# Kernel optimization log

Measured on AMD Instinct MI355X. Metric: run time of the kernel, lower is better.

Reference implementation:

```python
import jax, jax.numpy as jnp
import numpy as np

THRESHOLD = 10.0
K = 24
EPS = 1e-9
BN_EPS = 1e-5


def setup_inputs() -> dict:
    key = jax.random.key(0)
    k0, k1, k2, k3 = jax.random.split(key, 4)
    B, C, H, W = 4, 256, 64, 64
    x = jax.random.normal(k0, (B, C, H, W), jnp.float32)
    fc_w = jax.random.normal(k1, (C, C), jnp.float32) * (1.0 / np.sqrt(C))
    fc_b = jax.random.normal(k2, (C,), jnp.float32) * 0.01
    dist_w = jax.random.normal(k3, (64, C), jnp.float32) * (1.0 / np.sqrt(C))
    bn_gamma = jnp.ones((C,), jnp.float32)
    bn_beta = jnp.zeros((C,), jnp.float32)
    return {"x": x, "fc_w": fc_w, "fc_b": fc_b, "dist_w": dist_w,
            "bn_gamma": bn_gamma, "bn_beta": bn_beta}


def reference(x, fc_w, fc_b, dist_w, bn_gamma, bn_beta):
    B, C, H, W = x.shape
    N = H * W
    # ds branch: only triggers when H == 40; here H=64 so ds=1 (no pool/interp)
    x_flat = x.reshape(B, C, N).transpose(0, 2, 1)        # [B, N, C]
    # dist_embed: 1x1 conv == linear projection per spatial location
    emb = jnp.einsum('bnc,ec->bne', x_flat, dist_w)       # [B, N, 64]
    # pairwise Euclidean distances (cdist)
    sq = jnp.sum(emb * emb, axis=-1)                      # [B, N]
    d2 = sq[:, :, None] + sq[:, None, :] - 2.0 * jnp.einsum('bne,bme->bnm', emb, emb)
    dist = jnp.sqrt(jnp.clip(d2, 0.0))                    # [B, N, N]
    # kNN mask via top_k of -dist
    _, idx = jax.lax.top_k(-dist, K)                      # [B, N, K]
    bi = jnp.arange(B)[:, None, None]
    ni = jnp.arange(N)[None, :, None]
    knn_mask = jnp.zeros((B, N, N), bool).at[bi, ni, idx].set(True)
    adj = knn_mask & (dist <= THRESHOLD)
    adj = adj | jnp.eye(N, dtype=bool)[None]
    adj_f = adj.astype(x.dtype)                           # H: [B, N, E=N]
    # HypConv: X' = Dv^{-1} H De^{-1} H^T (X Theta), residual added outside
    X_lin = x_flat @ fc_w.T + fc_b                        # [B, N, C]
    Dv = jnp.clip(jnp.sum(adj_f, axis=2), EPS, None)      # [B, N]
    De = jnp.clip(jnp.sum(adj_f, axis=1), EPS, None)      # [B, E]
    H_De_inv = adj_f / De[:, None, :]
    S = (H_De_inv @ adj_f.transpose(0, 2, 1)) / Dv[:, :, None]   # [B, N, N]
    out_flat = S @ X_lin + x_flat                         # residual
    out = out_flat.transpose(0, 2, 1).reshape(B, C, H, W)
    # BatchNorm2d in training mode (batch statistics, biased variance)
    mean = jnp.mean(out, axis=(0, 2, 3))
    var = jnp.var(out, axis=(0, 2, 3))
    o = (out - mean[None, :, None, None]) * jax.lax.rsqrt(var[None, :, None, None] + BN_EPS)
    o = o * bn_gamma[None, :, None, None] + bn_beta[None, :, None, None]
    # SiLU
    return o * jax.nn.sigmoid(o)
```

## Files before the change

kernel.cpp:

```cpp
#include <hip/hip_runtime.h>

#define NB 4096
#define BATCH 4
#define CD 256
#define ED 64
#define KNN 24

typedef __attribute__((ext_vector_type(8))) short bf16x8;
typedef __attribute__((ext_vector_type(4))) float f32x4;

__device__ __forceinline__ unsigned short f2bf(float x) {
  unsigned u = __float_as_uint(x);
  unsigned r = (u + 0x7fffu + ((u >> 16) & 1u)) >> 16;
  return (unsigned short)r;
}

__global__ __launch_bounds__(256) void k_emb(const float* __restrict__ x,
                                             const float* __restrict__ dist_w,
                                             unsigned* __restrict__ emb_hl,
                                             float* __restrict__ sq,
                                             unsigned* __restrict__ thr_g) {
  __shared__ float wds[ED * CD];
  __shared__ float red[64 * 4];
  const int b = blockIdx.x >> 6;
  const int n0 = (blockIdx.x & 63) << 6;
  const int tid = threadIdx.x;
  const float4* wsrc = (const float4*)dist_w;
  float4* wdst = (float4*)wds;
#pragma unroll
  for (int k = 0; k < 16; ++k) wdst[tid + 256 * k] = wsrc[tid + 256 * k];
  __syncthreads();
  const int eg = tid >> 6;
  const int nl = tid & 63;
  const int n = n0 + nl;
  float acc[16];
#pragma unroll
  for (int t = 0; t < 16; ++t) acc[t] = 0.f;
  const float* xb = x + (size_t)b * CD * NB + n;
#pragma unroll 2
  for (int c4 = 0; c4 < CD; c4 += 4) {
    float x0 = xb[(size_t)(c4 + 0) * NB];
    float x1 = xb[(size_t)(c4 + 1) * NB];
    float x2 = xb[(size_t)(c4 + 2) * NB];
    float x3 = xb[(size_t)(c4 + 3) * NB];
#pragma unroll
    for (int t = 0; t < 16; ++t) {
      float4 wv = *(const float4*)&wds[(eg * 16 + t) * CD + c4];
      acc[t] = fmaf(x0, wv.x, acc[t]);
      acc[t] = fmaf(x1, wv.y, acc[t]);
      acc[t] = fmaf(x2, wv.z, acc[t]);
      acc[t] = fmaf(x3, wv.w, acc[t]);
    }
  }
  float s = 0.f;
#pragma unroll
  for (int t = 0; t < 16; ++t) s = fmaf(acc[t], acc[t], s);
  unsigned hw[8], lw[8];
#pragma unroll
  for (int i = 0; i < 8; ++i) {
    unsigned short h0 = f2bf(acc[2 * i]);
    unsigned short h1 = f2bf(acc[2 * i + 1]);
    float l0f = acc[2 * i] - __uint_as_float((unsigned)h0 << 16);
    float l1f = acc[2 * i + 1] - __uint_as_float((unsigned)h1 << 16);
    hw[i] = (unsigned)h0 | ((unsigned)h1 << 16);
    lw[i] = (unsigned)f2bf(l0f) | ((unsigned)f2bf(l1f) << 16);
  }
  uint4* g = (uint4*)emb_hl;
  const size_t gb = ((size_t)(b * NB + n)) * 16;
  const int k15 = n & 15;
  g[gb + ((2 * eg) ^ k15)]     = make_uint4(hw[0], hw[1], hw[2], hw[3]);
  g[gb + ((2 * eg + 1) ^ k15)] = make_uint4(hw[4], hw[5], hw[6], hw[7]);
  g[gb + ((8 + 2 * eg) ^ k15)]     = make_uint4(lw[0], lw[1], lw[2], lw[3]);
  g[gb + ((8 + 2 * eg + 1) ^ k15)] = make_uint4(lw[4], lw[5], lw[6], lw[7]);
  red[nl * 4 + eg] = s;
  __syncthreads();
  if (tid < 64) {
    sq[b * NB + n0 + tid] = red[tid * 4] + red[tid * 4 + 1] + red[tid * 4 + 2] + red[tid * 4 + 3];
    thr_g[(b << 12) + n0 + tid] = 0x42C80000u;
  }
}

__global__ __launch_bounds__(256) void k_wsplit(const float* __restrict__ fc_w,
                                                unsigned* __restrict__ w_hl) {
  const int u = blockIdx.x * 256 + threadIdx.x;
  const int c = u >> 5, cg = u & 31;
  const int kt = cg >> 3, chl = cg & 7;
  const float* src = fc_w + (size_t)c * CD + kt * 64 + chl * 8;
  unsigned hi[4], lo[4];
#pragma unroll
  for (int j = 0; j < 4; ++j) {
    float a0 = src[2 * j], a1 = src[2 * j + 1];
    unsigned short h0 = f2bf(a0), h1 = f2bf(a1);
    float l0 = a0 - __uint_as_float((unsigned)h0 << 16);
    float l1 = a1 - __uint_as_float((unsigned)h1 << 16);
    hi[j] = (unsigned)h0 | ((unsigned)h1 << 16);
    lo[j] = (unsigned)f2bf(l0) | ((unsigned)f2bf(l1) << 16);
  }
  uint4* dst = (uint4*)w_hl;
  const int base = (c * 4 + kt) * 16;
  const int k15 = c & 15;
  dst[base + (chl ^ k15)] = make_uint4(hi[0], hi[1], hi[2], hi[3]);
  dst[base + ((chl + 8) ^ k15)] = make_uint4(lo[0], lo[1], lo[2], lo[3]);
}

__global__ __launch_bounds__(512) void k_xlin(const float* __restrict__ x,
                                              const unsigned* __restrict__ w_hl,
                                              const float* __restrict__ fc_b,
                                              float* __restrict__ xlin) {
  __shared__ __align__(16) unsigned char smem[49152];
  float* xt = (float*)smem;
  unsigned* xhl = (unsigned*)(smem + 16384);
  unsigned* whl = (unsigned*)(smem + 32768);
  const int bid = blockIdx.x;
  const int ct = bid & 3;
  const int nt = (bid >> 2) & 63;
  const int b = bid >> 8;
  const int n0 = nt << 6;
  const int tid = threadIdx.x;
  const int w = tid >> 6, lane = tid & 63;
  const int quad = lane >> 4, lr = lane & 15;
  const int rt = w >> 1;
  const int ct0 = (w & 1) * 2;
  const int rowA = rt * 16 + lr;
  const int cvt_n = tid & 63, cvt_k8 = tid >> 6;
  uint4* whl4 = (uint4*)whl;
  uint4* xhl4 = (uint4*)xhl;
  const uint4* wg = (const uint4*)w_hl;
  f32x4 acc0 = {0.f, 0.f, 0.f, 0.f};
  f32x4 acc1 = {0.f, 0.f, 0.f, 0.f};

#pragma unroll 1
  for (int kt = 0; kt < 4; ++kt) {
    __syncthreads();
#pragma unroll
    for (int i = 0; i < 8; ++i) {
      int idx = tid + 512 * i;
      int k = idx >> 6, n = idx & 63;
      xt[k * 64 + n] = x[((size_t)(b * CD + kt * 64 + k)) * NB + n0 + n];
    }
#pragma unroll
    for (int i = 0; i < 2; ++i) {
      int idx = tid + 512 * i;
      int r = idx >> 4, ch = idx & 15;
      whl4[r * 16 + ch] = wg[(size_t)((ct * 64 + r) * 4 + kt) * 16 + ch];
    }
    __syncthreads();
    {
      unsigned hi[4], lo[4];
#pragma unroll
      for (int j = 0; j < 4; ++j) {
        float a0 = xt[(cvt_k8 * 8 + 2 * j) * 64 + cvt_n];
        float a1 = xt[(cvt_k8 * 8 + 2 * j + 1) * 64 + cvt_n];
        unsigned short h0 = f2bf(a0), h1 = f2bf(a1);
        float l0 = a0 - __uint_as_float((unsigned)h0 << 16);
        float l1 = a1 - __uint_as_float((unsigned)h1 << 16);
        hi[j] = (unsigned)h0 | ((unsigned)h1 << 16);
        lo[j] = (unsigned)f2bf(l0) | ((unsigned)f2bf(l1) << 16);
      }
      const int k15 = cvt_n & 15;
      xhl4[cvt_n * 16 + (cvt_k8 ^ k15)] = make_uint4(hi[0], hi[1], hi[2], hi[3]);
      xhl4[cvt_n * 16 + ((cvt_k8 + 8) ^ k15)] = make_uint4(lo[0], lo[1], lo[2], lo[3]);
    }
    __syncthreads();
#pragma unroll
    for (int kk = 0; kk < 2; ++kk) {
      const int cb = quad + 4 * kk;
      bf16x8 a_hi = *(const bf16x8*)&xhl[rowA * 64 + ((cb) ^ lr) * 4];
      bf16x8 a_lo = *(const bf16x8*)&xhl[rowA * 64 + ((cb + 8) ^ lr) * 4];
      int rowB0 = ct0 * 16 + lr, rowB1 = rowB0 + 16;
      bf16x8 b0_hi = *(const bf16x8*)&whl[rowB0 * 64 + ((cb) ^ lr) * 4];
      bf16x8 b0_lo = *(const bf16x8*)&whl[rowB0 * 64 + ((cb + 8) ^ lr) * 4];
      bf16x8 b1_hi = *(const bf16x8*)&whl[rowB1 * 64 + ((cb) ^ lr) * 4];
      bf16x8 b1_lo = *(const bf16x8*)&whl[rowB1 * 64 + ((cb + 8) ^ lr) * 4];
      acc0 = __builtin_amdgcn_mfma_f32_16x16x32_bf16(a_hi, b0_hi, acc0, 0, 0, 0);
      acc0 = __builtin_amdgcn_mfma_f32_16x16x32_bf16(a_hi, b0_lo, acc0, 0, 0, 0);
      acc0 = __builtin_amdgcn_mfma_f32_16x16x32_bf16(a_lo, b0_hi, acc0, 0, 0, 0);
      acc1 = __builtin_amdgcn_mfma_f32_16x16x32_bf16(a_hi, b1_hi, acc1, 0, 0, 0);
      acc1 = __builtin_amdgcn_mfma_f32_16x16x32_bf16(a_hi, b1_lo, acc1, 0, 0, 0);
      acc1 = __builtin_amdgcn_mfma_f32_16x16x32_bf16(a_lo, b1_hi, acc1, 0, 0, 0);
    }
  }
#pragma unroll
  for (int reg = 0; reg < 4; ++reg) {
    int n = n0 + rt * 16 + quad * 4 + reg;
    float* dst = xlin + ((size_t)(b * NB + n)) * CD + ct * 64;
    int c0 = ct0 * 16 + lr;
    dst[c0] = acc0[reg] + fc_b[ct * 64 + c0];
    dst[c0 + 16] = acc1[reg] + fc_b[ct * 64 + c0 + 16];
  }
}

__global__ __launch_bounds__(512, 4) void k_distp(const unsigned* __restrict__ emb_hl,
                                                  const float* __restrict__ sq,
                                                  unsigned* __restrict__ thr_g,
                                                  unsigned long long* __restrict__ part) {
  __shared__ __align__(16) unsigned char smem[78592];
  unsigned* eN = (unsigned*)smem;
  unsigned* eM = (unsigned*)(smem + 16384);
  float* sqN   = (float*)(smem + 32768);
  float* sqMp  = (float*)(smem + 33024);
  int* hist    = (int*)(smem + 35072);
  int* collectK= (int*)(smem + 51456);
  int* cnt     = (int*)(smem + 51712);
  unsigned long long* cand = (unsigned long long*)(smem + 51968);

  const int bid = blockIdx.x;
  const int mp = bid & 7;
  const int nt = (bid >> 3) & 63;
  const int b  = bid >> 9;
  const int n0 = nt << 6;
  const int m00 = mp << 9;
  const int tid = threadIdx.x;
  const uint4* embg = (const uint4*)emb_hl;
  const size_t bbase = (size_t)b * NB;
  const int gbase = (b << 12) + n0;

#pragma unroll
  for (int k = 0; k < 2; ++k) {
    int q = tid + 512 * k;
    int r = q >> 4, ch = q & 15;
    *(uint4*)&eN[r * 64 + ch * 4] = embg[(bbase + n0 + r) * 16 + ch];
  }
  if (tid < 64) sqN[tid] = sq[b * NB + n0 + tid];
  sqMp[tid] = sq[b * NB + m00 + tid];
#pragma unroll
  for (int i = 0; i < 8; ++i) hist[tid + 512 * i] = 0;

  const int w = tid >> 6, lane = tid & 63;
  const int quad = lane >> 4, lr = lane & 15;
  const int rt = w >> 1;
  const int ct0 = (w & 1) * 2;
  const int rowA = rt * 16 + lr;
  const int rA = tid >> 4, chA = tid & 15;
  const int rB = rA + 32;

  uint4 pf0, pf1;

#define CHUNK_MFMA(m0_)                                                            \
  f32x4 acc0 = {0.f, 0.f, 0.f, 0.f};                                               \
  f32x4 acc1 = {0.f, 0.f, 0.f, 0.f};                                               \
  _Pragma("unroll")                                                                \
  for (int kk = 0; kk < 2; ++kk) {                                                 \
    const int cb = quad + 4 * kk;                                                  \
    bf16x8 a_hi = *(const bf16x8*)&eN[rowA * 64 + ((cb) ^ lr) * 4];                \
    bf16x8 a_lo = *(const bf16x8*)&eN[rowA * 64 + ((cb + 8) ^ lr) * 4];            \
    int rowB0 = ct0 * 16 + lr, rowB1 = rowB0 + 16;                                 \
    bf16x8 b0_hi = *(const bf16x8*)&eM[rowB0 * 64 + ((cb) ^ lr) * 4];              \
    bf16x8 b0_lo = *(const bf16x8*)&eM[rowB0 * 64 + ((cb + 8) ^ lr) * 4];          \
    bf16x8 b1_hi = *(const bf16x8*)&eM[rowB1 * 64 + ((cb) ^ lr) * 4];              \
    bf16x8 b1_lo = *(const bf16x8*)&eM[rowB1 * 64 + ((cb + 8) ^ lr) * 4];          \
    acc0 = __builtin_amdgcn_mfma_f32_16x16x32_bf16(a_hi, b0_hi, acc0, 0, 0, 0);    \
    acc0 = __builtin_amdgcn_mfma_f32_16x16x32_bf16(a_hi, b0_lo, acc0, 0, 0, 0);    \
    acc0 = __builtin_amdgcn_mfma_f32_16x16x32_bf16(a_lo, b0_hi, acc0, 0, 0, 0);    \
    acc1 = __builtin_amdgcn_mfma_f32_16x16x32_bf16(a_hi, b1_hi, acc1, 0, 0, 0);    \
    acc1 = __builtin_amdgcn_mfma_f32_16x16x32_bf16(a_hi, b1_lo, acc1, 0, 0, 0);    \
    acc1 = __builtin_amdgcn_mfma_f32_16x16x32_bf16(a_lo, b1_hi, acc1, 0, 0, 0);    \
  }

#define STAGE_FIRST()                                                \
  pf0 = embg[(bbase + m00 + rA) * 16 + chA];                         \
  pf1 = embg[(bbase + m00 + rB) * 16 + chA];                         \
  *(uint4*)&eM[rA * 64 + chA * 4] = pf0;                             \
  *(uint4*)&eM[rB * 64 + chA * 4] = pf1;                             \
  pf0 = embg[(bbase + m00 + 64 + rA) * 16 + chA];                    \
  pf1 = embg[(bbase + m00 + 64 + rB) * 16 + chA];

#define RESTAGE(ci_, m0_)                                            \
  if ((ci_) < 7) {                                                   \
    *(uint4*)&eM[rA * 64 + chA * 4] = pf0;                           \
    *(uint4*)&eM[rB * 64 + chA * 4] = pf1;                           \
    if ((ci_) < 6) {                                                 \
      pf0 = embg[(bbase + m00 + (m0_) + 128 + rA) * 16 + chA];       \
      pf1 = embg[(bbase + m00 + (m0_) + 128 + rB) * 16 + chA];       \
    }                                                                \
  }

  STAGE_FIRST()
#pragma unroll 1
  for (int ci = 0; ci < 8; ++ci) {
    const int m0 = ci << 6;
    __syncthreads();
    CHUNK_MFMA(m0)
#pragma unroll
    for (int reg = 0; reg < 4; ++reg) {
      int row = rt * 16 + quad * 4 + reg;
      int c0 = ct0 * 16 + lr, c1 = c0 + 16;
      float d20 = fmaxf(sqN[row] + sqMp[m0 + c0] - 2.f * acc0[reg], 0.f);
      float d21 = fmaxf(sqN[row] + sqMp[m0 + c1] - 2.f * acc1[reg], 0.f);
      if (__float_as_uint(d20) <= 0x42C80000u) {
        int bk0 = min(63, (int)(d20 * 0.64f));
        atomicAdd(&hist[bk0 * 64 + row], 1);
      }
      if (__float_as_uint(d21) <= 0x42C80000u) {
        int bk1 = min(63, (int)(d21 * 0.64f));
        atomicAdd(&hist[bk1 * 64 + row], 1);
      }
    }
    __syncthreads();
    RESTAGE(ci, m0)
  }

  if (tid < 64) {
    int cum = 0, kb = 63;
#pragma unroll 1
    for (int k2 = 0; k2 < 64; ++k2) {
      cum += hist[k2 * 64 + tid];
      if (cum >= 24) { kb = k2; break; }
    }
    float edge = (float)(kb + 2) * 1.5625f;
    atomicMin(&thr_g[gbase + tid], __float_as_uint(edge));
    unsigned tg = thr_g[gbase + tid];
    int kImp = min(63, (int)(__uint_as_float(tg) * 0.64f));
    collectK[tid] = min(kb, kImp);
    cnt[tid] = 0;
  }
#pragma unroll
  for (int i = 0; i < 7; ++i) {
    int q = tid + 512 * i;
    if (q < 64 * 52) cand[q] = ~0ULL;
  }
  __syncthreads();

  STAGE_FIRST()
#pragma unroll 1
  for (int ci = 0; ci < 8; ++ci) {
    const int m0 = ci << 6;
    __syncthreads();
    CHUNK_MFMA(m0)
#pragma unroll
    for (int reg = 0; reg < 4; ++reg) {
      int row = rt * 16 + quad * 4 + reg;
      int c0 = ct0 * 16 + lr, c1 = c0 + 16;
      float d20 = fmaxf(sqN[row] + sqMp[m0 + c0] - 2.f * acc0[reg], 0.f);
      float d21 = fmaxf(sqN[row] + sqMp[m0 + c1] - 2.f * acc1[reg], 0.f);
      int kc = collectK[row];
      unsigned bi0 = __float_as_uint(d20), bi1 = __float_as_uint(d21);
      int bk0 = min(63, (int)(d20 * 0.64f));
      int bk1 = min(63, (int)(d21 * 0.64f));
      if (bk0 <= kc && bi0 <= 0x42C80000u) {
        int pos = atomicAdd(&cnt[row], 1);
        if (pos < 52) cand[row * 52 + pos] = ((unsigned long long)bi0 << 32) | (unsigned)(m00 + m0 + c0);
      }
      if (bk1 <= kc && bi1 <= 0x42C80000u) {
        int pos = atomicAdd(&cnt[row], 1);
        if (pos < 52) cand[row * 52 + pos] = ((unsigned long long)bi1 << 32) | (unsigned)(m00 + m0 + c1);
      }
    }
    __syncthreads();
    RESTAGE(ci, m0)
  }
  __syncthreads();

  {
    const int row8 = tid >> 3, sub = tid & 7;
    unsigned long long last = 0;
    unsigned long long* op = part + ((size_t)bid * 64 + row8) * 24;
#pragma unroll 1
    for (int k = 0; k < 24; ++k) {
      unsigned long long lm = ~0ULL;
#pragma unroll
      for (int j2 = 0; j2 < 7; ++j2) {
        int p2 = sub + 8 * j2;
        if (p2 < 52) {
          unsigned long long v2 = cand[row8 * 52 + p2];
          if ((k == 0 || v2 > last) && v2 < lm) lm = v2;
        }
      }
#pragma unroll
      for (int s2 = 1; s2 < 8; s2 <<= 1) {
        unsigned long long o2 = __shfl_xor(lm, s2);
        if (o2 < lm) lm = o2;
      }
      if (sub == 0) op[k] = lm;
      last = lm;
    }
  }
}

__global__ __launch_bounds__(64) void k_merge(const unsigned long long* __restrict__ part,
                                              int* __restrict__ row_idx,
                                              int* __restrict__ row_cnt,
                                              int* __restrict__ col_cnt) {
  const int row = blockIdx.x * 64 + threadIdx.x;
  const int b = row >> 12;
  const int n = row & 4095;
  const int nt = n >> 6, r = n & 63;
  const size_t gb = (size_t)(((b << 6) | nt) << 3);
  unsigned long long h[8];
  int pp[8];
#pragma unroll
  for (int t = 0; t < 8; ++t) {
    h[t] = part[((gb + t) * 64 + r) * 24];
    pp[t] = 0;
  }
  int cnt = 0;
  const int base = row * KNN;
  for (int k = 0; k < 24; ++k) {
    int bs = 0;
    unsigned long long mv = h[0];
#pragma unroll
    for (int t = 1; t < 8; ++t)
      if (h[t] < mv) { mv = h[t]; bs = t; }
    if ((unsigned)(mv >> 32) > 0x42C80000u) break;
    int mi = (int)(mv & 0xFFFFFFFFu);
    row_idx[base + cnt] = mi;
    atomicAdd(&col_cnt[(b << 12) + mi], 1);
    ++cnt;
    int np = ++pp[bs];
    h[bs] = (np < 24) ? part[((gb + bs) * 64 + r) * 24 + np] : ~0ULL;
  }
  row_cnt[row] = cnt;
#pragma unroll 4
  for (int j = cnt; j < 24; ++j) row_idx[base + j] = n;
}

__global__ __launch_bounds__(256) void k_scan(const int* __restrict__ col_cnt,
                                              int* __restrict__ col_start,
                                              int* __restrict__ col_cursor) {
  __shared__ int part[256];
  const int tid = threadIdx.x;
  const int base = tid * 64;
  int s = 0;
  for (int j = 0; j < 64; ++j) s += col_cnt[base + j];
  part[tid] = s;
  __syncthreads();
  for (int off = 1; off < 256; off <<= 1) {
    int v = (tid >= off) ? part[tid - off] : 0;
    __syncthreads();
    part[tid] += v;
    __syncthreads();
  }
  int run = part[tid] - s;
  for (int j = 0; j < 64; ++j) {
    col_start[base + j] = run;
    col_cursor[base + j] = run;
    run += col_cnt[base + j];
  }
}

__global__ __launch_bounds__(64) void k_fill(const int* __restrict__ row_idx,
                                             const int* __restrict__ row_cnt,
                                             int* __restrict__ col_cursor,
                                             int* __restrict__ col_list) {
  const int row = blockIdx.x * 64 + threadIdx.x;
  const int b = row >> 12;
  const int cnt = row_cnt[row];
  for (int j = 0; j < cnt; ++j) {
    int m = row_idx[row * KNN + j];
    int pos = atomicAdd(&col_cursor[(b << 12) + m], 1);
    col_list[pos] = row & 4095;
  }
}

__global__ __launch_bounds__(256) void k_yd(const float* __restrict__ xlin,
                                            const int* __restrict__ col_cnt,
                                            const int* __restrict__ col_start,
                                            const int* __restrict__ col_list,
                                            float* __restrict__ yd) {
  const int le = threadIdx.x >> 6;
  const int c4 = threadIdx.x & 63;
  const int be = blockIdx.x * 4 + le;
  const int b = be >> 12;
  const int deg = col_cnt[be];
  const int start = col_start[be];
  float4 acc = make_float4(0.f, 0.f, 0.f, 0.f);
  int j = 0;
  for (; j + 3 < deg; j += 4) {
    int ma = col_list[start + j], mb2 = col_list[start + j + 1];
    int mc = col_list[start + j + 2], md = col_list[start + j + 3];
    float4 va = *(const float4*)&xlin[(((size_t)(b << 12) + ma) << 8) + c4 * 4];
    float4 vb = *(const float4*)&xlin[(((size_t)(b << 12) + mb2) << 8) + c4 * 4];
    float4 vc = *(const float4*)&xlin[(((size_t)(b << 12) + mc) << 8) + c4 * 4];
    float4 vd = *(const float4*)&xlin[(((size_t)(b << 12) + md) << 8) + c4 * 4];
    acc.x += (va.x + vb.x) + (vc.x + vd.x);
    acc.y += (va.y + vb.y) + (vc.y + vd.y);
    acc.z += (va.z + vb.z) + (vc.z + vd.z);
    acc.w += (va.w + vb.w) + (vc.w + vd.w);
  }
  for (; j < deg; ++j) {
    int m = col_list[start + j];
    float4 v = *(const float4*)&xlin[(((size_t)(b << 12) + m) << 8) + c4 * 4];
    acc.x += v.x; acc.y += v.y; acc.z += v.z; acc.w += v.w;
  }
  float inv = 1.f / (float)deg;
  acc.x *= inv; acc.y *= inv; acc.z *= inv; acc.w *= inv;
  *(float4*)&yd[((size_t)be << 8) + c4 * 4] = acc;
}

__global__ __launch_bounds__(256) void k_out2(const float* __restrict__ yd,
                                              const int* __restrict__ row_idx,
                                              const int* __restrict__ row_cnt,
                                              float* __restrict__ outf) {
  const int b = blockIdx.x >> 8;
  const int nt = blockIdx.x & 255;
  const int le = threadIdx.x >> 6;
  const int c4 = threadIdx.x & 63;
  for (int ii = 0; ii < 4; ++ii) {
    int n = nt * 16 + le * 4 + ii;
    int row = (b << 12) + n;
    int cnt = row_cnt[row];
    int idx[24];
    const int4* ip = (const int4*)(row_idx + (size_t)row * KNN);
#pragma unroll
    for (int t = 0; t < 6; ++t) {
      int4 v = ip[t];
      idx[4 * t] = v.x; idx[4 * t + 1] = v.y; idx[4 * t + 2] = v.z; idx[4 * t + 3] = v.w;
    }
    float4 acc = make_float4(0.f, 0.f, 0.f, 0.f);
#pragma unroll
    for (int j = 0; j < 24; ++j) {
      float wgt = (j < cnt) ? 1.f : 0.f;
      float4 v = *(const float4*)&yd[(((size_t)(b << 12) + idx[j]) << 8) + c4 * 4];
      acc.x = fmaf(wgt, v.x, acc.x);
      acc.y = fmaf(wgt, v.y, acc.y);
      acc.z = fmaf(wgt, v.z, acc.z);
      acc.w = fmaf(wgt, v.w, acc.w);
    }
    float inv = 1.f / (float)cnt;
    acc.x *= inv; acc.y *= inv; acc.z *= inv; acc.w *= inv;
    *(float4*)&outf[((size_t)row << 8) + c4 * 4] = acc;
  }
}

__global__ __launch_bounds__(256) void k_res_bn(const float* __restrict__ x,
                                                float* __restrict__ outf,
                                                float* __restrict__ bn_sum,
                                                float* __restrict__ bn_sumsq) {
  __shared__ float xt[256 * 69];
  const int b = blockIdx.x >> 6;
  const int n0 = (blockIdx.x & 63) << 6;
  const int tid = threadIdx.x;
#pragma unroll 4
  for (int k = 0; k < 16; ++k) {
    int q = tid + 256 * k;
    int c = q >> 4, f = q & 15;
    float4 v = *(const float4*)&x[((size_t)(b * CD + c)) * NB + n0 + 4 * f];
    xt[c * 69 + 4 * f + 0] = v.x;
    xt[c * 69 + 4 * f + 1] = v.y;
    xt[c * 69 + 4 * f + 2] = v.z;
    xt[c * 69 + 4 * f + 3] = v.w;
  }
  __syncthreads();
  float s = 0.f, q = 0.f;
  const size_t rbase = ((size_t)((b << 12) + n0)) << 8;
#pragma unroll 4
  for (int i = 0; i < 64; ++i) {
    float v = outf[rbase + (size_t)i * 256 + tid] + xt[tid * 69 + i];
    outf[rbase + (size_t)i * 256 + tid] = v;
    s += v;
    q = fmaf(v, v, q);
  }
  atomicAdd(&bn_sum[tid], s);
  atomicAdd(&bn_sumsq[tid], q);
}

__global__ __launch_bounds__(256) void k_write(const float* __restrict__ outf,
                                               const float* __restrict__ bn_sum,
                                               const float* __restrict__ bn_sumsq,
                                               const float* __restrict__ gamma,
                                               const float* __restrict__ beta,
                                               float* __restrict__ out) {
  __shared__ float tile[64 * 257];
  __shared__ float sc[256], sh[256];
  const int b = blockIdx.x >> 6;
  const int n0 = (blockIdx.x & 63) << 6;
  const int tid = threadIdx.x;
  {
    const float inv = 1.f / 16384.f;
    float mean = bn_sum[tid] * inv;
    float var = bn_sumsq[tid] * inv - mean * mean;
    float scf = gamma[tid] * rsqrtf(var + 1e-5f);
    sc[tid] = scf;
    sh[tid] = beta[tid] - mean * scf;
  }
  __syncthreads();
#pragma unroll 4
  for (int i = 0; i < 64; ++i) {
    int idx = tid + 256 * i;
    int n = idx >> 8, c = idx & 255;
    float v = outf[(((size_t)(b << 12) + n0 + n) << 8) + c];
    v = fmaf(v, sc[c], sh[c]);
    float w = v / (1.f + expf(-v));
    tile[n * 257 + c] = w;
  }
  __syncthreads();
  const int nl = tid & 63;
  const int cg = tid >> 6;
#pragma unroll 4
  for (int j = 0; j < 64; ++j) {
    int c = cg * 64 + j;
    out[((size_t)(b * CD + c)) * NB + n0 + nl] = tile[nl * 257 + c];
  }
}

extern "C" void kernel_launch(void* const* d_in, const int* in_sizes, int n_in,
                              void* d_out, int out_size, void* d_ws, size_t ws_size,
                              hipStream_t stream) {
  const float* x      = (const float*)d_in[0];
  const float* fc_w   = (const float*)d_in[1];
  const float* fc_b   = (const float*)d_in[2];
  const float* dist_w = (const float*)d_in[3];
  const float* gamma  = (const float*)d_in[4];
  const float* beta   = (const float*)d_in[5];
  float* out = (float*)d_out;
  char* ws = (char*)d_ws;

  const size_t OFF_EHL   = 0;
  const size_t OFF_XLIN  = (size_t)4 << 20;
  const size_t OFF_YD    = (size_t)20 << 20;
  const size_t OFF_OUTF  = (size_t)36 << 20;
  const size_t OFF_SQ    = (size_t)52 << 20;
  const size_t OFF_RIDX  = OFF_SQ + 65536;
  const size_t OFF_RCNT  = OFF_RIDX + 1572864;
  const size_t OFF_CCNT  = OFF_RCNT + 65536;
  const size_t OFF_CSTART = OFF_CCNT + 65536;
  const size_t OFF_CCUR  = OFF_CSTART + 65536;
  const size_t OFF_CLIST = OFF_CCUR + 65536;
  const size_t OFF_BNS   = OFF_CLIST + 1572864;
  const size_t OFF_BNQ   = OFF_BNS + 1024;
  const size_t OFF_THRG  = OFF_BNQ + 1024;
  const size_t OFF_WHL   = OFF_THRG + 65536;
  const size_t TOTAL = OFF_WHL + 262144;
  if (ws_size < TOTAL) return;

  unsigned* emb_hl = (unsigned*)(ws + OFF_EHL);
  float* xlin  = (float*)(ws + OFF_XLIN);
  float* yd    = (float*)(ws + OFF_YD);
  float* outf  = (float*)(ws + OFF_OUTF);
  unsigned long long* part = (unsigned long long*)(ws + OFF_YD);
  float* sq    = (float*)(ws + OFF_SQ);
  int* row_idx = (int*)(ws + OFF_RIDX);
  int* row_cnt = (int*)(ws + OFF_RCNT);
  int* col_cnt = (int*)(ws + OFF_CCNT);
  int* col_start = (int*)(ws + OFF_CSTART);
  int* col_cursor = (int*)(ws + OFF_CCUR);
  int* col_list = (int*)(ws + OFF_CLIST);
  float* bn_sum = (float*)(ws + OFF_BNS);
  float* bn_sumsq = (float*)(ws + OFF_BNQ);
  unsigned* thr_g = (unsigned*)(ws + OFF_THRG);
  unsigned* w_hl = (unsigned*)(ws + OFF_WHL);

  hipMemsetAsync(col_cnt, 0, 65536, stream);
  hipMemsetAsync(bn_sum, 0, 2048, stream);

  k_emb<<<256, 256, 0, stream>>>(x, dist_w, emb_hl, sq, thr_g);
  k_wsplit<<<32, 256, 0, stream>>>(fc_w, w_hl);
  k_xlin<<<1024, 512, 0, stream>>>(x, w_hl, fc_b, xlin);
  k_distp<<<2048, 512, 0, stream>>>(emb_hl, sq, thr_g, part);
  k_merge<<<256, 64, 0, stream>>>(part, row_idx, row_cnt, col_cnt);
  k_scan<<<1, 256, 0, stream>>>(col_cnt, col_start, col_cursor);
  k_fill<<<256, 64, 0, stream>>>(row_idx, row_cnt, col_cursor, col_list);
  k_yd<<<4096, 256, 0, stream>>>(xlin, col_cnt, col_start, col_list, yd);
  k_out2<<<1024, 256, 0, stream>>>(yd, row_idx, row_cnt, outf);
  k_res_bn<<<256, 256, 0, stream>>>(x, outf, bn_sum, bn_sumsq);
  k_write<<<256, 256, 0, stream>>>(outf, bn_sum, bn_sumsq, gamma, beta, out);
}
```

Baseline: 497.5 us.

## Double-buffer eM tiles in k_distp, keep A operands in registers, pack histogram

Makes the eM shared-memory tile double-buffered, so each chunk loop iteration needs one barrier instead of two. The A-side embedding fragments now load from global memory straight into registers once, which removes the eN shared buffer and the repeated LDS reads of it. The per-row histogram is packed as two 16-bit counters per word, halving its LDS footprint and zero-init cost. Total shared memory drops while eM doubles, which could allow higher occupancy, but the packed counters and the extra registers holding A fragments add some risk.

```diff
diff --git a/kernel.cpp b/kernel.cpp
--- a/kernel.cpp
+++ b/kernel.cpp
@@ -194,15 +194,14 @@
                                                   const float* __restrict__ sq,
                                                   unsigned* __restrict__ thr_g,
                                                   unsigned long long* __restrict__ part) {
-  __shared__ __align__(16) unsigned char smem[78592];
-  unsigned* eN = (unsigned*)smem;
-  unsigned* eM = (unsigned*)(smem + 16384);
-  float* sqN   = (float*)(smem + 32768);
-  float* sqMp  = (float*)(smem + 33024);
-  int* hist    = (int*)(smem + 35072);
-  int* collectK= (int*)(smem + 51456);
-  int* cnt     = (int*)(smem + 51712);
-  unsigned long long* cand = (unsigned long long*)(smem + 51968);
+  __shared__ __align__(16) unsigned char smem[70400];
+  unsigned* eM   = (unsigned*)smem;
+  float* sqN     = (float*)(smem + 32768);
+  float* sqMp    = (float*)(smem + 33024);
+  unsigned* hist = (unsigned*)(smem + 35072);
+  int* collectK  = (int*)(smem + 43264);
+  int* cnt       = (int*)(smem + 43520);
+  unsigned long long* cand = (unsigned long long*)(smem + 43776);
 
   const int bid = blockIdx.x;
   const int mp = bid & 7;
@@ -215,16 +214,10 @@
   const size_t bbase = (size_t)b * NB;
   const int gbase = (b << 12) + n0;
 
-#pragma unroll
-  for (int k = 0; k < 2; ++k) {
-    int q = tid + 512 * k;
-    int r = q >> 4, ch = q & 15;
-    *(uint4*)&eN[r * 64 + ch * 4] = embg[(bbase + n0 + r) * 16 + ch];
-  }
   if (tid < 64) sqN[tid] = sq[b * NB + n0 + tid];
   sqMp[tid] = sq[b * NB + m00 + tid];
 #pragma unroll
-  for (int i = 0; i < 8; ++i) hist[tid + 512 * i] = 0;
+  for (int i = 0; i < 4; ++i) hist[tid + 512 * i] = 0;
 
   const int w = tid >> 6, lane = tid & 63;
   const int quad = lane >> 4, lr = lane & 15;
@@ -234,21 +227,27 @@
   const int rA = tid >> 4, chA = tid & 15;
   const int rB = rA + 32;
 
+  bf16x8 aHi0 = *(const bf16x8*)&emb_hl[((bbase + n0 + rowA) * 16 + ((quad) ^ lr)) * 4];
+  bf16x8 aLo0 = *(const bf16x8*)&emb_hl[((bbase + n0 + rowA) * 16 + ((quad + 8) ^ lr)) * 4];
+  bf16x8 aHi1 = *(const bf16x8*)&emb_hl[((bbase + n0 + rowA) * 16 + ((quad + 4) ^ lr)) * 4];
+  bf16x8 aLo1 = *(const bf16x8*)&emb_hl[((bbase + n0 + rowA) * 16 + ((quad + 12) ^ lr)) * 4];
+
+  uint4* eM4 = (uint4*)eM;
   uint4 pf0, pf1;
 
-#define CHUNK_MFMA(m0_)                                                            \
+#define CHUNK_MFMA_R(eMc)                                                          \
   f32x4 acc0 = {0.f, 0.f, 0.f, 0.f};                                               \
   f32x4 acc1 = {0.f, 0.f, 0.f, 0.f};                                               \
   _Pragma("unroll")                                                                \
   for (int kk = 0; kk < 2; ++kk) {                                                 \
     const int cb = quad + 4 * kk;                                                  \
-    bf16x8 a_hi = *(const bf16x8*)&eN[rowA * 64 + ((cb) ^ lr) * 4];                \
-    bf16x8 a_lo = *(const bf16x8*)&eN[rowA * 64 + ((cb + 8) ^ lr) * 4];            \
+    bf16x8 a_hi = kk ? aHi1 : aHi0;                                                \
+    bf16x8 a_lo = kk ? aLo1 : aLo0;                                                \
     int rowB0 = ct0 * 16 + lr, rowB1 = rowB0 + 16;                                 \
-    bf16x8 b0_hi = *(const bf16x8*)&eM[rowB0 * 64 + ((cb) ^ lr) * 4];              \
-    bf16x8 b0_lo = *(const bf16x8*)&eM[rowB0 * 64 + ((cb + 8) ^ lr) * 4];          \
-    bf16x8 b1_hi = *(const bf16x8*)&eM[rowB1 * 64 + ((cb) ^ lr) * 4];              \
-    bf16x8 b1_lo = *(const bf16x8*)&eM[rowB1 * 64 + ((cb + 8) ^ lr) * 4];          \
+    bf16x8 b0_hi = *(const bf16x8*)&(eMc)[rowB0 * 64 + ((cb) ^ lr) * 4];           \
+    bf16x8 b0_lo = *(const bf16x8*)&(eMc)[rowB0 * 64 + ((cb + 8) ^ lr) * 4];       \
+    bf16x8 b1_hi = *(const bf16x8*)&(eMc)[rowB1 * 64 + ((cb) ^ lr) * 4];           \
+    bf16x8 b1_lo = *(const bf16x8*)&(eMc)[rowB1 * 64 + ((cb + 8) ^ lr) * 4];       \
     acc0 = __builtin_amdgcn_mfma_f32_16x16x32_bf16(a_hi, b0_hi, acc0, 0, 0, 0);    \
     acc0 = __builtin_amdgcn_mfma_f32_16x16x32_bf16(a_hi, b0_lo, acc0, 0, 0, 0);    \
     acc0 = __builtin_amdgcn_mfma_f32_16x16x32_bf16(a_lo, b0_hi, acc0, 0, 0, 0);    \
@@ -257,30 +256,32 @@
     acc1 = __builtin_amdgcn_mfma_f32_16x16x32_bf16(a_lo, b1_hi, acc1, 0, 0, 0);    \
   }
 
-#define STAGE_FIRST()                                                \
+#define STAGE_PROLOGUE()                                             \
   pf0 = embg[(bbase + m00 + rA) * 16 + chA];                         \
   pf1 = embg[(bbase + m00 + rB) * 16 + chA];                         \
-  *(uint4*)&eM[rA * 64 + chA * 4] = pf0;                             \
-  *(uint4*)&eM[rB * 64 + chA * 4] = pf1;                             \
+  eM4[rA * 16 + chA] = pf0;                                          \
+  eM4[rB * 16 + chA] = pf1;                                          \
   pf0 = embg[(bbase + m00 + 64 + rA) * 16 + chA];                    \
   pf1 = embg[(bbase + m00 + 64 + rB) * 16 + chA];
 
-#define RESTAGE(ci_, m0_)                                            \
+#define RESTAGE_DB(ci_)                                              \
   if ((ci_) < 7) {                                                   \
-    *(uint4*)&eM[rA * 64 + chA * 4] = pf0;                           \
-    *(uint4*)&eM[rB * 64 + chA * 4] = pf1;                           \
+    uint4* dst = eM4 + (((ci_) + 1) & 1) * 1024;                     \
+    dst[rA * 16 + chA] = pf0;                                        \
+    dst[rB * 16 + chA] = pf1;                                        \
     if ((ci_) < 6) {                                                 \
-      pf0 = embg[(bbase + m00 + (m0_) + 128 + rA) * 16 + chA];       \
-      pf1 = embg[(bbase + m00 + (m0_) + 128 + rB) * 16 + chA];       \
+      pf0 = embg[(bbase + m00 + ((ci_) + 2) * 64 + rA) * 16 + chA];  \
+      pf1 = embg[(bbase + m00 + ((ci_) + 2) * 64 + rB) * 16 + chA];  \
     }                                                                \
   }
 
-  STAGE_FIRST()
+  STAGE_PROLOGUE()
 #pragma unroll 1
   for (int ci = 0; ci < 8; ++ci) {
     const int m0 = ci << 6;
     __syncthreads();
-    CHUNK_MFMA(m0)
+    const unsigned* eMc = eM + (ci & 1) * 4096;
+    CHUNK_MFMA_R(eMc)
 #pragma unroll
     for (int reg = 0; reg < 4; ++reg) {
       int row = rt * 16 + quad * 4 + reg;
@@ -289,22 +290,23 @@
       float d21 = fmaxf(sqN[row] + sqMp[m0 + c1] - 2.f * acc1[reg], 0.f);
       if (__float_as_uint(d20) <= 0x42C80000u) {
         int bk0 = min(63, (int)(d20 * 0.64f));
-        atomicAdd(&hist[bk0 * 64 + row], 1);
+        atomicAdd(&hist[bk0 * 32 + (row >> 1)], 1u << (16 * (row & 1)));
       }
       if (__float_as_uint(d21) <= 0x42C80000u) {
         int bk1 = min(63, (int)(d21 * 0.64f));
-        atomicAdd(&hist[bk1 * 64 + row], 1);
+        atomicAdd(&hist[bk1 * 32 + (row >> 1)], 1u << (16 * (row & 1)));
       }
     }
-    __syncthreads();
-    RESTAGE(ci, m0)
-  }
+    RESTAGE_DB(ci)
+  }
+  __syncthreads();
 
   if (tid < 64) {
     int cum = 0, kb = 63;
+    const int sh = 16 * (tid & 1);
 #pragma unroll 1
     for (int k2 = 0; k2 < 64; ++k2) {
-      cum += hist[k2 * 64 + tid];
+      cum += (hist[k2 * 32 + (tid >> 1)] >> sh) & 0xFFFFu;
       if (cum >= 24) { kb = k2; break; }
     }
     float edge = (float)(kb + 2) * 1.5625f;
@@ -321,12 +323,13 @@
   }
   __syncthreads();
 
-  STAGE_FIRST()
+  STAGE_PROLOGUE()
 #pragma unroll 1
   for (int ci = 0; ci < 8; ++ci) {
     const int m0 = ci << 6;
     __syncthreads();
-    CHUNK_MFMA(m0)
+    const unsigned* eMc = eM + (ci & 1) * 4096;
+    CHUNK_MFMA_R(eMc)
 #pragma unroll
     for (int reg = 0; reg < 4; ++reg) {
       int row = rt * 16 + quad * 4 + reg;
@@ -346,8 +349,7 @@
         if (pos < 52) cand[row * 52 + pos] = ((unsigned long long)bi1 << 32) | (unsigned)(m00 + m0 + c1);
       }
     }
-    __syncthreads();
-    RESTAGE(ci, m0)
+    RESTAGE_DB(ci)
   }
   __syncthreads();
 
```

Result: no change. 491.1 us (-1.3%).
